# Kernel optimization log

Measured on AMD Instinct MI355X. Metric: run time of the kernel, lower is better.

Reference implementation:

```python
import jax, jax.numpy as jnp
import numpy as np

E = 8          # n_experts
K = 5          # n_active = int(0.7*E)
TEMP = float(np.e)

def _l2norm(v):
    n = jnp.linalg.norm(v, axis=-1, keepdims=True)
    return v / jnp.maximum(n, 1e-12)

def setup_inputs() -> dict:
    key = jax.random.key(0)
    ks = jax.random.split(key, 13)
    N, D, H, O = 4096, 2048, 4096, 2048
    s = lambda fan: 1.0 / np.sqrt(fan)
    return {
        "x":    jax.random.normal(ks[0], (N, D), jnp.float32),
        "Wg":   jax.random.normal(ks[1], (D, E), jnp.float32) * s(D),
        "bg":   jnp.zeros((E,), jnp.float32),
        "Wa":   jax.random.normal(ks[2], (D, 32), jnp.float32) * s(D),
        "ba":   jnp.zeros((32,), jnp.float32),
        "Wb":   jax.random.normal(ks[3], (32, 16), jnp.float32) * s(32),
        "bb":   jnp.zeros((16,), jnp.float32),
        "sigs": jax.random.normal(ks[4], (E, 16), jnp.float32) * 0.1,
        "W1":   jax.random.normal(ks[5], (E, D, H), jnp.float32) * s(D),
        "b1":   jnp.zeros((E, H), jnp.float32),
        "W2":   jax.random.normal(ks[6], (E, H, O), jnp.float32) * s(H),
        "b2":   jnp.zeros((E, O), jnp.float32),
    }

def reference(x, Wg, bg, Wa, ba, Wb, bb, sigs, W1, b1, W2, b2):
    # gating softmax (temperature = e)
    probs = jax.nn.softmax((x @ Wg + bg) / TEMP, axis=-1)          # [N, E]
    # PH feature match
    ph = jax.nn.relu(x @ Wa + ba) @ Wb + bb                        # [N, 16]
    ph_match = (_l2norm(ph) @ _l2norm(sigs).T + 1.0) / 2.0         # [N, E]
    effective = probs * ph_match                                   # [N, E]
    # top-k mask over experts
    _, idx = jax.lax.top_k(effective, K)                           # [N, K]
    mask = jnp.sum(jax.nn.one_hot(idx, E, dtype=effective.dtype), axis=-2)  # [N, E]
    weights = effective * mask
    weights = weights / (weights.sum(axis=-1, keepdims=True) + 1e-8)
    # dense all-expert FFN (eval mode: dropout is identity)
    h = jax.nn.relu(jnp.einsum('nd,edh->neh', x, W1) + b1)         # [N, E, H]
    outs = jnp.einsum('neh,eho->neo', h, W2) + b2                  # [N, E, O]
    return jnp.einsum('ne,neo->no', weights, outs)                 # [N, O]
```

## Files before the change

### kernel.cpp

```cpp
#include <hip/hip_runtime.h>
#include <hip/hip_bf16.h>
#include <stdint.h>

#define TOK  4096
#define DIM  2048
#define HID  4096
#define ODIM 2048
#define NEXP 8
#define KSEL 5
#define KTOT (NEXP * HID)

typedef __bf16 bf16x8 __attribute__((ext_vector_type(8)));
typedef float  f32x4  __attribute__((ext_vector_type(4)));

__device__ __forceinline__ uint16_t f2bf(float f) {
  uint32_t u = __float_as_uint(f);
  u += 0x7FFFu + ((u >> 16) & 1u);
  return (uint16_t)(u >> 16);
}

#define GLD16(g, l) __builtin_amdgcn_global_load_lds(                      \
    (const __attribute__((address_space(1))) void*)(g),                    \
    (__attribute__((address_space(3))) void*)(l), 16, 0, 0)


__global__ void cast_x_kernel(const float* __restrict__ in,
                              uint16_t* __restrict__ out, int n4) {
  int i = blockIdx.x * blockDim.x + threadIdx.x;
  if (i >= n4) return;
  float4 v = ((const float4*)in)[i];
  ushort4 o;
  o.x = f2bf(v.x); o.y = f2bf(v.y); o.z = f2bf(v.z); o.w = f2bf(v.w);
  ((ushort4*)out)[i] = o;
}

__global__ void transpose_cast_kernel(const float* __restrict__ in,
                                      uint16_t* __restrict__ out,
                                      int R, int C, long inBatch, long outBatch) {
  __shared__ float tile[32][33];
  const float* src = in + (size_t)blockIdx.z * inBatch;
  uint16_t*    dst = out + (size_t)blockIdx.z * outBatch;
  int c0 = blockIdx.x * 32, r0 = blockIdx.y * 32;
  int tx = threadIdx.x, ty = threadIdx.y;
#pragma unroll
  for (int i = 0; i < 4; ++i)
    tile[ty + i * 8][tx] = src[(size_t)(r0 + ty + i * 8) * C + c0 + tx];
  __syncthreads();
#pragma unroll
  for (int i = 0; i < 4; ++i)
    dst[(size_t)(c0 + ty + i * 8) * R + r0 + tx] = f2bf(tile[tx][ty + i * 8]);
}


__global__ void routing_kernel(const float* __restrict__ x,
                               const float* __restrict__ Wg, const float* __restrict__ bg,
                               const float* __restrict__ Wa, const float* __restrict__ ba,
                               const float* __restrict__ Wb, const float* __restrict__ bb,
                               const float* __restrict__ sigs,
                               float* __restrict__ wts) {
  const int n    = blockIdx.x;
  const int lane = threadIdx.x;
  const float* xr = x + (size_t)n * DIM;

  float ga[NEXP]; float aa[32];
#pragma unroll
  for (int e = 0; e < NEXP; ++e) ga[e] = 0.f;
#pragma unroll
  for (int j = 0; j < 32; ++j) aa[j] = 0.f;

  for (int it = 0; it < DIM / 64; ++it) {
    int d = it * 64 + lane;
    float xv = xr[d];
    const float* wgr = Wg + (size_t)d * NEXP;
#pragma unroll
    for (int e = 0; e < NEXP; ++e) ga[e] += xv * wgr[e];
    const float* war = Wa + (size_t)d * 32;
#pragma unroll
    for (int j = 0; j < 32; ++j) aa[j] += xv * war[j];
  }
#pragma unroll
  for (int s = 1; s < 64; s <<= 1) {
#pragma unroll
    for (int e = 0; e < NEXP; ++e) ga[e] += __shfl_xor(ga[e], s);
#pragma unroll
    for (int j = 0; j < 32; ++j) aa[j] += __shfl_xor(aa[j], s);
  }

  float ph[16];
#pragma unroll
  for (int i = 0; i < 16; ++i) ph[i] = bb[i];
#pragma unroll
  for (int j = 0; j < 32; ++j) {
    float a = aa[j] + ba[j];
    a = a > 0.f ? a : 0.f;
#pragma unroll
    for (int i = 0; i < 16; ++i) ph[i] += a * Wb[j * 16 + i];
  }
  float nrm = 0.f;
#pragma unroll
  for (int i = 0; i < 16; ++i) nrm += ph[i] * ph[i];
  nrm = fmaxf(sqrtf(nrm), 1e-12f);

  const float invT = 0.36787944117144233f;
  float lg[NEXP], mx = -1e30f;
#pragma unroll
  for (int e = 0; e < NEXP; ++e) { lg[e] = (ga[e] + bg[e]) * invT; mx = fmaxf(mx, lg[e]); }
  float psum = 0.f, pr[NEXP];
#pragma unroll
  for (int e = 0; e < NEXP; ++e) { pr[e] = expf(lg[e] - mx); psum += pr[e]; }

  float eff[NEXP];
#pragma unroll
  for (int e = 0; e < NEXP; ++e) {
    const float* sg = sigs + e * 16;
    float dot = 0.f, sn = 0.f;
#pragma unroll
    for (int i = 0; i < 16; ++i) { dot += ph[i] * sg[i]; sn += sg[i] * sg[i]; }
    sn = fmaxf(sqrtf(sn), 1e-12f);
    float match = (dot / (nrm * sn) + 1.f) * 0.5f;
    eff[e] = (pr[e] / psum) * match;
  }

  int selmask = 0;
#pragma unroll
  for (int t = 0; t < KSEL; ++t) {
    int bi = 0; float bv = -1e30f;
#pragma unroll
    for (int e = 0; e < NEXP; ++e) {
      bool ok = !((selmask >> e) & 1);
      if (ok && eff[e] > bv) { bv = eff[e]; bi = e; }
    }
    selmask |= (1 << bi);
  }
  float wsum = 0.f, wv[NEXP];
#pragma unroll
  for (int e = 0; e < NEXP; ++e) {
    wv[e] = ((selmask >> e) & 1) ? eff[e] : 0.f;
    wsum += wv[e];
  }
  float inv = 1.f / (wsum + 1e-8f);
  if (lane == 0) {
#pragma unroll
    for (int e = 0; e < NEXP; ++e) wts[n * NEXP + e] = wv[e] * inv;
  }
}


template <int MODE>
__global__ void gemm_bt_kernel(const uint16_t* __restrict__ A,
                               const uint16_t* __restrict__ Bt,
                               int M, int Nloc, int K,
                               const float* __restrict__ wts,
                               const float* __restrict__ bias,
                               uint16_t* __restrict__ outBf,
                               float* __restrict__ outF) {
  __shared__ __attribute__((aligned(16))) uint16_t smA[128 * 64];
  __shared__ __attribute__((aligned(16))) uint16_t smB[128 * 64];
  const int e     = blockIdx.z;
  const uint16_t* Bte = Bt + (size_t)e * Nloc * K;
  const int tileM = blockIdx.y * 128;
  const int tileN = blockIdx.x * 128;
  const int tid  = threadIdx.x;
  const int lane = tid & 63;
  const int wid  = tid >> 6;
  const int wr = wid >> 1, wc = wid & 1;

  f32x4 acc[4][4];
#pragma unroll
  for (int m = 0; m < 4; ++m)
#pragma unroll
    for (int n = 0; n < 4; ++n)
      acc[m][n] = (f32x4){0.f, 0.f, 0.f, 0.f};

  for (int k0 = 0; k0 < K; k0 += 64) {
#pragma unroll
    for (int j = 0; j < 4; ++j) {
      const int f   = (wid * 4 + j) * 64 + lane;
      const int row = f >> 3;
      const int s8  = (f & 7) ^ (row & 7);
      GLD16(A   + (size_t)(tileM + row) * K + k0 + s8 * 8, (char*)smA + (wid * 4 + j) * 1024);
      GLD16(Bte + (size_t)(tileN + row) * K + k0 + s8 * 8, (char*)smB + (wid * 4 + j) * 1024);
    }
    __syncthreads();

#pragma unroll
    for (int kk = 0; kk < 2; ++kk) {
      bf16x8 av[4], bv[4];
#pragma unroll
      for (int m = 0; m < 4; ++m) {
        const int row = wr * 64 + m * 16 + (lane & 15);
        const int g   = (kk * 4 + (lane >> 4)) ^ (row & 7);
        av[m] = *(const bf16x8*)(smA + row * 64 + g * 8);
      }
#pragma unroll
      for (int n = 0; n < 4; ++n) {
        const int row = wc * 64 + n * 16 + (lane & 15);
        const int g   = (kk * 4 + (lane >> 4)) ^ (row & 7);
        bv[n] = *(const bf16x8*)(smB + row * 64 + g * 8);
      }
#pragma unroll
      for (int m = 0; m < 4; ++m)
#pragma unroll
        for (int n = 0; n < 4; ++n)
          acc[m][n] = __builtin_amdgcn_mfma_f32_16x16x32_bf16(av[m], bv[n], acc[m][n], 0, 0, 0);
    }
    __syncthreads();
  }

  if (MODE == 1) {
    float wv[4][4];
#pragma unroll
    for (int m = 0; m < 4; ++m)
#pragma unroll
      for (int r = 0; r < 4; ++r) {
        const int row = tileM + wr * 64 + m * 16 + ((lane >> 4) << 2) + r;
        wv[m][r] = wts[row * NEXP + e];
      }
    const float* be = bias + (size_t)e * Nloc;
#pragma unroll
    for (int n = 0; n < 4; ++n) {
      const int col  = tileN + wc * 64 + n * 16 + (lane & 15);
      const float bc = be[col];
#pragma unroll
      for (int m = 0; m < 4; ++m)
#pragma unroll
        for (int r = 0; r < 4; ++r) {
          const int row = tileM + wr * 64 + m * 16 + ((lane >> 4) << 2) + r;
          float v = acc[m][n][r] + bc;
          v = v > 0.f ? v : 0.f;
          v *= wv[m][r];
          outBf[(size_t)row * KTOT + (size_t)e * HID + col] = f2bf(v);
        }
    }
  } else {
#pragma unroll
    for (int m = 0; m < 4; ++m)
#pragma unroll
      for (int r = 0; r < 4; ++r) {
        const int row = tileM + wr * 64 + m * 16 + ((lane >> 4) << 2) + r;
        const float* w8 = wts + row * NEXP;
        float w[8];
#pragma unroll
        for (int q = 0; q < 8; ++q) w[q] = w8[q];
#pragma unroll
        for (int n = 0; n < 4; ++n) {
          const int col = tileN + wc * 64 + n * 16 + (lane & 15);
          float s = acc[m][n][r];
#pragma unroll
          for (int q = 0; q < 8; ++q) s += w[q] * bias[q * ODIM + col];
          outF[(size_t)row * ODIM + col] = s;
        }
      }
  }
}


extern "C" void kernel_launch(void* const* d_in, const int* in_sizes, int n_in,
                              void* d_out, int out_size, void* d_ws, size_t ws_size,
                              hipStream_t stream) {
  const float* x    = (const float*)d_in[0];
  const float* Wg   = (const float*)d_in[1];
  const float* bg   = (const float*)d_in[2];
  const float* Wa   = (const float*)d_in[3];
  const float* ba   = (const float*)d_in[4];
  const float* Wb   = (const float*)d_in[5];
  const float* bb   = (const float*)d_in[6];
  const float* sigs = (const float*)d_in[7];
  const float* W1   = (const float*)d_in[8];
  const float* b1   = (const float*)d_in[9];
  const float* W2   = (const float*)d_in[10];
  const float* b2   = (const float*)d_in[11];
  float* out = (float*)d_out;

  char* ws = (char*)d_ws;
  float*    wts  = (float*)(ws + 0);
  uint16_t* xbf  = (uint16_t*)(ws + 131072);
  uint16_t* W1T  = (uint16_t*)(ws + 16908288);
  uint16_t* W2T  = (uint16_t*)(ws + 151126016);
  uint16_t* hbuf = (uint16_t*)(ws + 285343744);

  cast_x_kernel<<<(TOK * DIM / 4) / 256, 256, 0, stream>>>(x, xbf, TOK * DIM / 4);
  transpose_cast_kernel<<<dim3(HID / 32, DIM / 32, NEXP), dim3(32, 8), 0, stream>>>(
      W1, W1T, DIM, HID, (long)DIM * HID, (long)DIM * HID);
  transpose_cast_kernel<<<dim3(ODIM / 32, KTOT / 32, 1), dim3(32, 8), 0, stream>>>(
      W2, W2T, KTOT, ODIM, 0, 0);
  routing_kernel<<<TOK, 64, 0, stream>>>(x, Wg, bg, Wa, ba, Wb, bb, sigs, wts);

  gemm_bt_kernel<1><<<dim3(HID / 128, TOK / 128, NEXP), 256, 0, stream>>>(
      xbf, W1T, TOK, HID, DIM, wts, b1, hbuf, nullptr);
  gemm_bt_kernel<2><<<dim3(ODIM / 128, TOK / 128, 1), 256, 0, stream>>>(
      hbuf, W2T, TOK, ODIM, KTOT, wts, b2, nullptr, out);
}
```

Baseline: 1.604 ms.

## Route tokens sparsely to selected experts instead of dense all-expert FFN

Measured after the change: 1.951 ms. 21.7% more time.

```diff
diff --git a/kernel.cpp b/kernel.cpp
--- a/kernel.cpp
+++ b/kernel.cpp
@@ -9,6 +9,7 @@
 #define NEXP 8
 #define KSEL 5
 #define KTOT (NEXP * HID)
+#define MAXROWS 21504
 
 typedef __bf16 bf16x8 __attribute__((ext_vector_type(8)));
 typedef float  f32x4  __attribute__((ext_vector_type(4)));
@@ -22,6 +23,40 @@
 #define GLD16(g, l) __builtin_amdgcn_global_load_lds(                      \
     (const __attribute__((address_space(1))) void*)(g),                    \
     (__attribute__((address_space(3))) void*)(l), 16, 0, 0)
+
+
+__global__ void zero_cnt_kernel(int* __restrict__ cnt) {
+  if (threadIdx.x < NEXP) cnt[threadIdx.x] = 0;
+}
+
+__global__ void scan_kernel(const int* __restrict__ cnt, int* __restrict__ base) {
+  if (threadIdx.x == 0) {
+    int r = 0;
+    for (int e = 0; e < NEXP; ++e) { base[e] = r; r += cnt[e]; }
+  }
+}
+
+__global__ void bias_init_kernel(const float* __restrict__ wts,
+                                 const float* __restrict__ b2,
+                                 float* __restrict__ out) {
+  const int n = blockIdx.x;
+  const int t = threadIdx.x;
+  float w[NEXP];
+#pragma unroll
+  for (int e = 0; e < NEXP; ++e) w[e] = wts[n * NEXP + e];
+#pragma unroll
+  for (int g = 0; g < 2; ++g) {
+    const int c = g * 1024 + t * 4;
+    float4 s = make_float4(0.f, 0.f, 0.f, 0.f);
+#pragma unroll
+    for (int e = 0; e < NEXP; ++e) {
+      const float4 bv = *(const float4*)(b2 + (size_t)e * ODIM + c);
+      s.x += w[e] * bv.x; s.y += w[e] * bv.y;
+      s.z += w[e] * bv.z; s.w += w[e] * bv.w;
+    }
+    *(float4*)(out + (size_t)n * ODIM + c) = s;
+  }
+}
 
 
 __global__ void cast_x_kernel(const float* __restrict__ in,
@@ -57,7 +92,8 @@
                                const float* __restrict__ Wa, const float* __restrict__ ba,
                                const float* __restrict__ Wb, const float* __restrict__ bb,
                                const float* __restrict__ sigs,
-                               float* __restrict__ wts) {
+                               float* __restrict__ wts,
+                               int* __restrict__ cnt, int* __restrict__ list) {
   const int n    = blockIdx.x;
   const int lane = threadIdx.x;
   const float* xr = x + (size_t)n * DIM;
@@ -142,47 +178,62 @@
   if (lane == 0) {
 #pragma unroll
     for (int e = 0; e < NEXP; ++e) wts[n * NEXP + e] = wv[e] * inv;
-  }
-}
-
-
-template <int MODE>
-__global__ void gemm_bt_kernel(const uint16_t* __restrict__ A,
-                               const uint16_t* __restrict__ Bt,
-                               int M, int Nloc, int K,
-                               const float* __restrict__ wts,
-                               const float* __restrict__ bias,
-                               uint16_t* __restrict__ outBf,
-                               float* __restrict__ outF) {
+#pragma unroll
+    for (int e = 0; e < NEXP; ++e) {
+      if ((selmask >> e) & 1) {
+        int p = atomicAdd(&cnt[e], 1);
+        list[e * TOK + p] = n;
+      }
+    }
+  }
+}
+
+
+__global__ void gemm1_kernel(const uint16_t* __restrict__ xbf,
+                             const uint16_t* __restrict__ W1T,
+                             const int* __restrict__ cnt,
+                             const int* __restrict__ base,
+                             const int* __restrict__ list,
+                             const float* __restrict__ wts,
+                             const float* __restrict__ b1,
+                             uint16_t* __restrict__ hbuf) {
   __shared__ __attribute__((aligned(16))) uint16_t smA[128 * 64];
   __shared__ __attribute__((aligned(16))) uint16_t smB[128 * 64];
-  const int e     = blockIdx.z;
-  const uint16_t* Bte = Bt + (size_t)e * Nloc * K;
+  const int e  = blockIdx.z;
+  const int ce = cnt[e];
   const int tileM = blockIdx.y * 128;
+  if (tileM >= ce) return;
+  const int be    = base[e];
   const int tileN = blockIdx.x * 128;
-  const int tid  = threadIdx.x;
-  const int lane = tid & 63;
-  const int wid  = tid >> 6;
+  const int tid = threadIdx.x, lane = tid & 63, wid = tid >> 6;
   const int wr = wid >> 1, wc = wid & 1;
+  const int* liste = list + e * TOK;
+
+  const uint16_t* srcA[4]; const uint16_t* srcB[4]; uint32_t lof[4];
+#pragma unroll
+  for (int j = 0; j < 4; ++j) {
+    const int f   = (wid * 4 + j) * 64 + lane;
+    const int row = f >> 3;
+    const int s8  = (f & 7) ^ (row & 7);
+    int p = tileM + row; p = p < ce ? p : ce - 1;
+    srcA[j] = xbf + (size_t)liste[p] * DIM + s8 * 8;
+    srcB[j] = W1T + ((size_t)e * HID + tileN + row) * DIM + s8 * 8;
+    lof[j]  = (wid * 4 + j) * 1024;
+  }
 
   f32x4 acc[4][4];
 #pragma unroll
   for (int m = 0; m < 4; ++m)
 #pragma unroll
-    for (int n = 0; n < 4; ++n)
-      acc[m][n] = (f32x4){0.f, 0.f, 0.f, 0.f};
-
-  for (int k0 = 0; k0 < K; k0 += 64) {
+    for (int n = 0; n < 4; ++n) acc[m][n] = (f32x4){0.f, 0.f, 0.f, 0.f};
+
+  for (int k0 = 0; k0 < DIM; k0 += 64) {
 #pragma unroll
     for (int j = 0; j < 4; ++j) {
-      const int f   = (wid * 4 + j) * 64 + lane;
-      const int row = f >> 3;
-      const int s8  = (f & 7) ^ (row & 7);
-      GLD16(A   + (size_t)(tileM + row) * K + k0 + s8 * 8, (char*)smA + (wid * 4 + j) * 1024);
-      GLD16(Bte + (size_t)(tileN + row) * K + k0 + s8 * 8, (char*)smB + (wid * 4 + j) * 1024);
+      GLD16(srcA[j] + k0, (char*)smA + lof[j]);
+      GLD16(srcB[j] + k0, (char*)smB + lof[j]);
     }
     __syncthreads();
-
 #pragma unroll
     for (int kk = 0; kk < 2; ++kk) {
       bf16x8 av[4], bv[4];
@@ -207,51 +258,109 @@
     __syncthreads();
   }
 
-  if (MODE == 1) {
-    float wv[4][4];
-#pragma unroll
-    for (int m = 0; m < 4; ++m)
-#pragma unroll
-      for (int r = 0; r < 4; ++r) {
-        const int row = tileM + wr * 64 + m * 16 + ((lane >> 4) << 2) + r;
-        wv[m][r] = wts[row * NEXP + e];
-      }
-    const float* be = bias + (size_t)e * Nloc;
-#pragma unroll
-    for (int n = 0; n < 4; ++n) {
-      const int col  = tileN + wc * 64 + n * 16 + (lane & 15);
-      const float bc = be[col];
+  const float* b1e = b1 + (size_t)e * HID;
+#pragma unroll
+  for (int m = 0; m < 4; ++m)
+#pragma unroll
+    for (int r = 0; r < 4; ++r) {
+      const int p = tileM + wr * 64 + m * 16 + ((lane >> 4) << 2) + r;
+      if (p < ce) {
+        const int n = liste[p];
+        const float w = wts[n * NEXP + e];
+        uint16_t* orow = hbuf + (size_t)(be + p) * HID;
+#pragma unroll
+        for (int nf = 0; nf < 4; ++nf) {
+          const int col = tileN + wc * 64 + nf * 16 + (lane & 15);
+          float v = acc[m][nf][r] + b1e[col];
+          v = v > 0.f ? v : 0.f;
+          orow[col] = f2bf(v * w);
+        }
+      }
+    }
+}
+
+
+__global__ void gemm2_kernel(const uint16_t* __restrict__ hbuf,
+                             const uint16_t* __restrict__ W2T,
+                             const int* __restrict__ cnt,
+                             const int* __restrict__ base,
+                             const int* __restrict__ list,
+                             float* __restrict__ out) {
+  __shared__ __attribute__((aligned(16))) uint16_t smA[128 * 64];
+  __shared__ __attribute__((aligned(16))) uint16_t smB[128 * 64];
+  const int e  = blockIdx.z;
+  const int ce = cnt[e];
+  const int tileM = blockIdx.y * 128;
+  if (tileM >= ce) return;
+  const int be    = base[e];
+  const int tileN = blockIdx.x * 128;
+  const int tid = threadIdx.x, lane = tid & 63, wid = tid >> 6;
+  const int wr = wid >> 1, wc = wid & 1;
+  const int* liste = list + e * TOK;
+
+  const uint16_t* srcA[4]; const uint16_t* srcB[4]; uint32_t lof[4];
+#pragma unroll
+  for (int j = 0; j < 4; ++j) {
+    const int f   = (wid * 4 + j) * 64 + lane;
+    const int row = f >> 3;
+    const int s8  = (f & 7) ^ (row & 7);
+    srcA[j] = hbuf + (size_t)(be + tileM + row) * HID + s8 * 8;
+    srcB[j] = W2T + (size_t)(tileN + row) * KTOT + e * HID + s8 * 8;
+    lof[j]  = (wid * 4 + j) * 1024;
+  }
+
+  f32x4 acc[4][4];
+#pragma unroll
+  for (int m = 0; m < 4; ++m)
+#pragma unroll
+    for (int n = 0; n < 4; ++n) acc[m][n] = (f32x4){0.f, 0.f, 0.f, 0.f};
+
+  for (int k0 = 0; k0 < HID; k0 += 64) {
+#pragma unroll
+    for (int j = 0; j < 4; ++j) {
+      GLD16(srcA[j] + k0, (char*)smA + lof[j]);
+      GLD16(srcB[j] + k0, (char*)smB + lof[j]);
+    }
+    __syncthreads();
+#pragma unroll
+    for (int kk = 0; kk < 2; ++kk) {
+      bf16x8 av[4], bv[4];
+#pragma unroll
+      for (int m = 0; m < 4; ++m) {
+        const int row = wr * 64 + m * 16 + (lane & 15);
+        const int g   = (kk * 4 + (lane >> 4)) ^ (row & 7);
+        av[m] = *(const bf16x8*)(smA + row * 64 + g * 8);
+      }
+#pragma unroll
+      for (int n = 0; n < 4; ++n) {
+        const int row = wc * 64 + n * 16 + (lane & 15);
+        const int g   = (kk * 4 + (lane >> 4)) ^ (row & 7);
+        bv[n] = *(const bf16x8*)(smB + row * 64 + g * 8);
+      }
 #pragma unroll
       for (int m = 0; m < 4; ++m)
 #pragma unroll
-        for (int r = 0; r < 4; ++r) {
-          const int row = tileM + wr * 64 + m * 16 + ((lane >> 4) << 2) + r;
-          float v = acc[m][n][r] + bc;
-          v = v > 0.f ? v : 0.f;
-          v *= wv[m][r];
-          outBf[(size_t)row * KTOT + (size_t)e * HID + col] = f2bf(v);
+        for (int n = 0; n < 4; ++n)
+          acc[m][n] = __builtin_amdgcn_mfma_f32_16x16x32_bf16(av[m], bv[n], acc[m][n], 0, 0, 0);
+    }
+    __syncthreads();
+  }
+
+#pragma unroll
+  for (int m = 0; m < 4; ++m)
+#pragma unroll
+    for (int r = 0; r < 4; ++r) {
+      const int p = tileM + wr * 64 + m * 16 + ((lane >> 4) << 2) + r;
+      if (p < ce) {
+        const int n = liste[p];
+        float* orow = out + (size_t)n * ODIM;
+#pragma unroll
+        for (int nf = 0; nf < 4; ++nf) {
+          const int col = tileN + wc * 64 + nf * 16 + (lane & 15);
+          atomicAdd(orow + col, acc[m][nf][r]);
         }
-    }
-  } else {
-#pragma unroll
-    for (int m = 0; m < 4; ++m)
-#pragma unroll
-      for (int r = 0; r < 4; ++r) {
-        const int row = tileM + wr * 64 + m * 16 + ((lane >> 4) << 2) + r;
-        const float* w8 = wts + row * NEXP;
-        float w[8];
-#pragma unroll
-        for (int q = 0; q < 8; ++q) w[q] = w8[q];
-#pragma unroll
-        for (int n = 0; n < 4; ++n) {
-          const int col = tileN + wc * 64 + n * 16 + (lane & 15);
-          float s = acc[m][n][r];
-#pragma unroll
-          for (int q = 0; q < 8; ++q) s += w[q] * bias[q * ODIM + col];
-          outF[(size_t)row * ODIM + col] = s;
-        }
-      }
-  }
+      }
+    }
 }
 
 
@@ -274,20 +383,26 @@
 
   char* ws = (char*)d_ws;
   float*    wts  = (float*)(ws + 0);
-  uint16_t* xbf  = (uint16_t*)(ws + 131072);
-  uint16_t* W1T  = (uint16_t*)(ws + 16908288);
-  uint16_t* W2T  = (uint16_t*)(ws + 151126016);
-  uint16_t* hbuf = (uint16_t*)(ws + 285343744);
-
+  int*      cnt  = (int*)(ws + 131072);
+  int*      base = (int*)(ws + 131104);
+  int*      list = (int*)(ws + 135168);
+  uint16_t* xbf  = (uint16_t*)(ws + 266240);
+  uint16_t* W1T  = (uint16_t*)(ws + 17043456);
+  uint16_t* W2T  = (uint16_t*)(ws + 151261184);
+  uint16_t* hbuf = (uint16_t*)(ws + 285478912);
+
+  zero_cnt_kernel<<<1, 64, 0, stream>>>(cnt);
   cast_x_kernel<<<(TOK * DIM / 4) / 256, 256, 0, stream>>>(x, xbf, TOK * DIM / 4);
   transpose_cast_kernel<<<dim3(HID / 32, DIM / 32, NEXP), dim3(32, 8), 0, stream>>>(
       W1, W1T, DIM, HID, (long)DIM * HID, (long)DIM * HID);
   transpose_cast_kernel<<<dim3(ODIM / 32, KTOT / 32, 1), dim3(32, 8), 0, stream>>>(
       W2, W2T, KTOT, ODIM, 0, 0);
-  routing_kernel<<<TOK, 64, 0, stream>>>(x, Wg, bg, Wa, ba, Wb, bb, sigs, wts);
-
-  gemm_bt_kernel<1><<<dim3(HID / 128, TOK / 128, NEXP), 256, 0, stream>>>(
-      xbf, W1T, TOK, HID, DIM, wts, b1, hbuf, nullptr);
-  gemm_bt_kernel<2><<<dim3(ODIM / 128, TOK / 128, 1), 256, 0, stream>>>(
-      hbuf, W2T, TOK, ODIM, KTOT, wts, b2, nullptr, out);
-}
+  routing_kernel<<<TOK, 64, 0, stream>>>(x, Wg, bg, Wa, ba, Wb, bb, sigs, wts, cnt, list);
+  scan_kernel<<<1, 64, 0, stream>>>(cnt, base);
+  bias_init_kernel<<<TOK, 256, 0, stream>>>(wts, b2, out);
+
+  gemm1_kernel<<<dim3(HID / 128, TOK / 128, NEXP), 256, 0, stream>>>(
+      xbf, W1T, cnt, base, list, wts, b1, hbuf);
+  gemm2_kernel<<<dim3(ODIM / 128, TOK / 128, NEXP), 256, 0, stream>>>(
+      hbuf, W2T, cnt, base, list, out);
+}
```
